# Performance work log

Hardware: AMD Instinct MI355X
Metric: run time of the kernel (lower is better)

## Reference

```python
import jax, jax.numpy as jnp
import numpy as np

HIDDEN = 1024

def setup_inputs() -> dict:
    key = jax.random.key(0)
    ks = jax.random.split(key, 7)
    B, S, H = 4, 2048, HIDDEN
    scale = 1.0 / np.sqrt(H)
    x = jax.random.normal(ks[0], (B, S, H), dtype=jnp.float32)
    Wq = jax.random.normal(ks[1], (H, H), dtype=jnp.float32) * scale
    Wk = jax.random.normal(ks[2], (H, H), dtype=jnp.float32) * scale
    Wv = jax.random.normal(ks[3], (H, H), dtype=jnp.float32) * scale
    bq = jax.random.normal(ks[4], (H,), dtype=jnp.float32) * 0.01
    bk = jax.random.normal(ks[5], (H,), dtype=jnp.float32) * 0.01
    bv = jax.random.normal(ks[6], (H,), dtype=jnp.float32) * 0.01
    return {"x": x, "Wq": Wq, "bq": bq, "Wk": Wk, "bk": bk, "Wv": Wv, "bv": bv}

def reference(x, Wq, bq, Wk, bk, Wv, bv):
    H = x.shape[-1]
    # Linear layers: y = x @ W^T + b (torch convention)
    Q = jnp.einsum('bsh,oh->bso', x, Wq) + bq
    K = jnp.einsum('bsh,oh->bso', x, Wk) + bk
    V = jnp.einsum('bsh,oh->bso', x, Wv) + bv
    # full O(S^2) score matrix, scaled by sqrt(hidden_dim) as in the source
    scores = jnp.einsum('bqh,bkh->bqk', Q, K) / jnp.sqrt(jnp.asarray(H, x.dtype))
    weights = jax.nn.softmax(scores, axis=-1)  # dropout is identity at inference
    out = jnp.einsum('bqk,bkh->bqh', weights, V)
    return out
```

## Files before the change

kernel.cpp:

```cpp
#include <hip/hip_runtime.h>
#include <hip/hip_bf16.h>

typedef __attribute__((ext_vector_type(8))) short bf16x8;
typedef __attribute__((ext_vector_type(4))) float f32x4;
typedef unsigned short u16;
typedef unsigned int u32;


__device__ __forceinline__ u16 f2bf(float f) {
  union { float f; u32 u; } v; v.f = f;
  u32 r = v.u + 0x7FFFu + ((v.u >> 16) & 1u);
  return (u16)(r >> 16);
}

__device__ __forceinline__ void gload_lds16(const u16* g, u16* l) {
  __builtin_amdgcn_global_load_lds(
      (const __attribute__((address_space(1))) u32*)(const void*)g,
      (__attribute__((address_space(3))) u32*)(void*)l, 16, 0, 0);
}


__global__ __launch_bounds__(256) void cvt_all(const float* __restrict__ x,
                                               const float* __restrict__ wq,
                                               const float* __restrict__ wk,
                                               const float* __restrict__ wv,
                                               u16* __restrict__ xb,
                                               u16* __restrict__ wcat) {
  const int bid = blockIdx.x;
  const float* src; u16* dst; size_t base;
  if (bid < 4096) { src = x; dst = xb; base = (size_t)bid * 2048; }
  else {
    int w = bid - 4096, s = w >> 9;
    src = (s == 0) ? wq : ((s == 1) ? wk : wv);
    dst = wcat + (size_t)s * 1048576;
    base = (size_t)(w & 511) * 2048;
  }
  size_t i = base + (size_t)threadIdx.x * 8;
  const float4* p = (const float4*)(src + i);
  float4 a = p[0], b = p[1];
  union { u16 u[8]; uint4 v; } r;
  r.u[0] = f2bf(a.x); r.u[1] = f2bf(a.y); r.u[2] = f2bf(a.z); r.u[3] = f2bf(a.w);
  r.u[4] = f2bf(b.x); r.u[5] = f2bf(b.y); r.u[6] = f2bf(b.z); r.u[7] = f2bf(b.w);
  *(uint4*)(dst + i) = r.v;
}


template<int MODE, int BM, int BN>
__global__ __launch_bounds__(512, 2) void gemm_pipe(
    const u16* __restrict__ A, const u16* __restrict__ B,
    const float* __restrict__ b0, const float* __restrict__ b1,
    const float* __restrict__ b2,
    void* __restrict__ o0, void* __restrict__ o1, void* __restrict__ o2,
    float* __restrict__ lsum, int lda, int ldb, int nkt,
    long Abat, long Bbat) {
  extern __shared__ u16 lds[];
  constexpr int NMT = BM / 32;
  constexpr int ANL = BM / 64;
  constexpr int BNL = BN / 64;
  constexpr int ASZ = BM * 64, BSZ = BN * 64;

  const int tid = threadIdx.x;
  const int lane = tid & 63, wv = tid >> 6;
  const int lr = lane & 15, lg = lane >> 4;
  const int wm = wv >> 2, wn = wv & 3;
  const int bm = blockIdx.x * BM, bn = blockIdx.y * BN;
  const int bz = blockIdx.z;

  const u16* Ab; const u16* Bb;
  if constexpr (MODE == 3) {
    Ab = A;
    Bb = B + (size_t)Bbat * (bm >> 11);
  } else {
    Ab = A + (size_t)Abat * bz;
    Bb = B + (size_t)Bbat * bz;
  }

  f32x4 acc[NMT][4];
#pragma unroll
  for (int i = 0; i < NMT; ++i)
#pragma unroll
    for (int j = 0; j < 4; ++j) acc[i][j] = (f32x4)0.0f;

  auto stage = [&](int kt, int buf) {
    u16* As = lds + buf * (ASZ + BSZ);
    u16* Bs = As + ASZ;
    const int k0 = kt * 64;
#pragma unroll
    for (int j = 0; j < ANL; ++j) {
      int id = j * 512 + tid, row = id >> 3, c = id & 7, cg = c ^ (row & 7);
      gload_lds16(Ab + (size_t)(bm + row) * lda + k0 + cg * 8, As + id * 8);
    }
#pragma unroll
    for (int j = 0; j < BNL; ++j) {
      int id = j * 512 + tid, row = id >> 3, c = id & 7, cg = c ^ (row & 7);
      gload_lds16(Bb + (size_t)(bn + row) * ldb + k0 + cg * 8, Bs + id * 8);
    }
  };

  stage(0, 0);
  __syncthreads();

  for (int kt = 0; kt < nkt; ++kt) {
    if (kt + 1 < nkt) stage(kt + 1, (kt + 1) & 1);
    __builtin_amdgcn_sched_barrier(0);
    const u16* As = lds + (kt & 1) * (ASZ + BSZ);
    const u16* Bs = As + ASZ;
#pragma unroll
    for (int kk = 0; kk < 2; ++kk) {
      bf16x8 a[NMT], b[4];
#pragma unroll
      for (int mt = 0; mt < NMT; ++mt) {
        int row = wm * (BM / 2) + mt * 16 + lr;
        int kc = (kk * 4 + lg) ^ (row & 7);
        a[mt] = *(const bf16x8*)(As + row * 64 + kc * 8);
      }
#pragma unroll
      for (int nt = 0; nt < 4; ++nt) {
        int row = wn * 64 + nt * 16 + lr;
        int kc = (kk * 4 + lg) ^ (row & 7);
        b[nt] = *(const bf16x8*)(Bs + row * 64 + kc * 8);
      }
#pragma unroll
      for (int mt = 0; mt < NMT; ++mt)
#pragma unroll
        for (int nt = 0; nt < 4; ++nt)
          acc[mt][nt] = __builtin_amdgcn_mfma_f32_16x16x32_bf16(a[mt], b[nt], acc[mt][nt], 0, 0, 0);
    }
    __syncthreads();
  }

  if constexpr (MODE == 0) {
    const int sel = bn >> 10;
    if (sel < 2) {
      const float* bp = sel ? b1 : b0;
      u16* o = sel ? (u16*)o1 : (u16*)o0;
#pragma unroll
      for (int nt = 0; nt < 4; ++nt) {
        int gcol = bn + wn * 64 + nt * 16 + lr;
        int col = gcol & 1023;
        float bv = bp[col];
#pragma unroll
        for (int mt = 0; mt < NMT; ++mt) {
          int grow0 = bm + wm * (BM / 2) + mt * 16 + lg * 4;
#pragma unroll
          for (int r = 0; r < 4; ++r)
            o[(size_t)(grow0 + r) * 1024 + col] = f2bf(acc[mt][nt][r] + bv);
        }
      }
    } else {
      u16* T = lds;
      const int col0 = bn - 2048;
      const int batch = bm >> 11;
      const int sbase = bm & 2047;
#pragma unroll
      for (int nt = 0; nt < 4; ++nt) {
        int col = wn * 64 + nt * 16 + lr;
        float bv = b2[col0 + col];
#pragma unroll
        for (int mt = 0; mt < NMT; ++mt) {
          int row0 = wm * (BM / 2) + mt * 16 + lg * 4;
#pragma unroll
          for (int r = 0; r < 4; ++r) {
            int row = row0 + r;
            T[row * 256 + (col ^ (((row >> 2) & 7) << 3))] = f2bf(acc[mt][nt][r] + bv);
          }
        }
      }
      __syncthreads();
      u16* o = (u16*)o2 + ((size_t)batch * 1024 + col0) * 2048 + sbase;
#pragma unroll
      for (int it = 0; it < 16; ++it) {
        int col = wv * 32 + (lane >> 2) + (it & 1) * 16;
        int s0 = ((it >> 1) * 4 + (lane & 3)) * 8;
        union { u16 u[8]; uint4 v; } pk;
#pragma unroll
        for (int k = 0; k < 8; ++k) {
          int row = s0 + k;
          pk.u[k] = T[row * 256 + (col ^ (((row >> 2) & 7) << 3))];
        }
        *(uint4*)(o + (size_t)col * 2048 + s0) = pk.v;
      }
    }
  } else if constexpr (MODE == 2) {
    u16* P = (u16*)o0 + (size_t)2048 * 2048 * bz;
    float psum[NMT][4];
#pragma unroll
    for (int mt = 0; mt < NMT; ++mt)
#pragma unroll
      for (int r = 0; r < 4; ++r) psum[mt][r] = 0.0f;
#pragma unroll
    for (int nt = 0; nt < 4; ++nt) {
      int gcol = bn + wn * 64 + nt * 16 + lr;
#pragma unroll
      for (int mt = 0; mt < NMT; ++mt) {
        int grow0 = bm + wm * (BM / 2) + mt * 16 + lg * 4;
#pragma unroll
        for (int r = 0; r < 4; ++r) {
          float e = __expf(acc[mt][nt][r] * 0.03125f);
          P[(size_t)(grow0 + r) * 2048 + gcol] = f2bf(e);
          psum[mt][r] += e;
        }
      }
    }
#pragma unroll
    for (int mt = 0; mt < NMT; ++mt)
#pragma unroll
      for (int r = 0; r < 4; ++r) {
#pragma unroll
        for (int off = 1; off < 16; off <<= 1)
          psum[mt][r] += __shfl_xor(psum[mt][r], off);
      }
    if (lr == 0) {
#pragma unroll
      for (int mt = 0; mt < NMT; ++mt) {
        int grow0 = bm + wm * (BM / 2) + mt * 16 + lg * 4;
#pragma unroll
        for (int r = 0; r < 4; ++r)
          atomicAdd(&lsum[bz * 2048 + grow0 + r], psum[mt][r]);
      }
    }
  } else {
    float* o = (float*)o0;
#pragma unroll
    for (int mt = 0; mt < NMT; ++mt) {
      int grow0 = bm + wm * (BM / 2) + mt * 16 + lg * 4;
      float inv[4];
#pragma unroll
      for (int r = 0; r < 4; ++r) inv[r] = 1.0f / lsum[grow0 + r];
#pragma unroll
      for (int nt = 0; nt < 4; ++nt) {
        int gcol = bn + wn * 64 + nt * 16 + lr;
#pragma unroll
        for (int r = 0; r < 4; ++r)
          o[(size_t)(grow0 + r) * 1024 + gcol] = acc[mt][nt][r] * inv[r];
      }
    }
  }
}


extern "C" void kernel_launch(void* const* d_in, const int* in_sizes, int n_in,
                              void* d_out, int out_size, void* d_ws, size_t ws_size,
                              hipStream_t stream) {
  const float* x  = (const float*)d_in[0];
  const float* Wq = (const float*)d_in[1];
  const float* bq = (const float*)d_in[2];
  const float* Wk = (const float*)d_in[3];
  const float* bk = (const float*)d_in[4];
  const float* Wv = (const float*)d_in[5];
  const float* bv = (const float*)d_in[6];
  float* out = (float*)d_out;

  char* ws = (char*)d_ws;
  u16*   xb   = (u16*)  (ws + ((size_t)0  << 20));
  u16*   wcat = (u16*)  (ws + ((size_t)16 << 20));
  float* lvec = (float*)(ws + ((size_t)23 << 20));
  u16*   qb   = (u16*)  (ws + ((size_t)24 << 20));
  u16*   kb   = (u16*)  (ws + ((size_t)40 << 20));
  u16*   vtb  = (u16*)  (ws + ((size_t)56 << 20));
  u16*   Pb   = (u16*)  (ws + ((size_t)72 << 20));

  hipFuncSetAttribute((const void*)&gemm_pipe<0, 256, 256>,
                      hipFuncAttributeMaxDynamicSharedMemorySize, 131072);
  hipFuncSetAttribute((const void*)&gemm_pipe<2, 256, 256>,
                      hipFuncAttributeMaxDynamicSharedMemorySize, 131072);
  hipFuncSetAttribute((const void*)&gemm_pipe<3, 128, 256>,
                      hipFuncAttributeMaxDynamicSharedMemorySize, 98304);

  hipMemsetAsync(lvec, 0, 8192 * sizeof(float), stream);
  cvt_all<<<dim3(5632), dim3(256), 0, stream>>>(x, Wq, Wk, Wv, xb, wcat);

  gemm_pipe<0, 256, 256><<<dim3(32, 12, 1), dim3(512), 131072, stream>>>(
      xb, wcat, bq, bk, bv, qb, kb, vtb, nullptr, 1024, 1024, 16, 0, 0);

  gemm_pipe<2, 256, 256><<<dim3(8, 8, 4), dim3(512), 131072, stream>>>(
      qb, kb, nullptr, nullptr, nullptr, Pb, nullptr, nullptr, lvec,
      1024, 1024, 16, (long)2048 * 1024, (long)2048 * 1024);

  gemm_pipe<3, 128, 256><<<dim3(64, 4, 1), dim3(512), 98304, stream>>>(
      Pb, vtb, nullptr, nullptr, nullptr, out, nullptr, nullptr, lvec,
      2048, 2048, 32, 0, (long)1024 * 2048);
}
```

Baseline: 246.1 us.

## Restructure GEMM main loop into eight-phase interleaved load/MFMA pipeline

Replaces the double-buffered GEMM loop with a finer schedule. Each 64-wide K tile is split into two 32-wide half slots, and the next tile's A and B loads are issued in four pieces interleaved with MFMA phases over two halves of the M tile. Explicit vmcnt/lgkmcnt waits, raw s_barrier and s_setprio replace the per-tile __syncthreads, so global-to-LDS copies overlap with matrix math. The LDS layout drops the XOR swizzle in favour of 32-element rows, which may bring back bank conflicts, and the hand-tuned waitcnt counts are fragile.

Result: slower. 269.7 us (+9.6%).

```diff
diff --git a/kernel.cpp b/kernel.cpp
--- a/kernel.cpp
+++ b/kernel.cpp
@@ -45,8 +45,8 @@
 }
 
 
-template<int MODE, int BM, int BN>
-__global__ __launch_bounds__(512, 2) void gemm_pipe(
+template<int MODE, int BM>
+__global__ __launch_bounds__(512, 2) void gemm8(
     const u16* __restrict__ A, const u16* __restrict__ B,
     const float* __restrict__ b0, const float* __restrict__ b1,
     const float* __restrict__ b2,
@@ -54,79 +54,109 @@
     float* __restrict__ lsum, int lda, int ldb, int nkt,
     long Abat, long Bbat) {
   extern __shared__ u16 lds[];
-  constexpr int NMT = BM / 32;
-  constexpr int ANL = BM / 64;
-  constexpr int BNL = BN / 64;
-  constexpr int ASZ = BM * 64, BSZ = BN * 64;
+  constexpr int MT = BM / 64;
+  constexpr int ASLOT = BM * 32;
+  constexpr int BSLOT = 256 * 32;
+  constexpr int BUFSZ = 2 * ASLOT + 2 * BSLOT;
+  constexpr int ALD = BM / 128;
 
   const int tid = threadIdx.x;
   const int lane = tid & 63, wv = tid >> 6;
   const int lr = lane & 15, lg = lane >> 4;
   const int wm = wv >> 2, wn = wv & 3;
-  const int bm = blockIdx.x * BM, bn = blockIdx.y * BN;
+  const int bm = blockIdx.x * BM, bn = blockIdx.y * 256;
   const int bz = blockIdx.z;
 
   const u16* Ab; const u16* Bb;
-  if constexpr (MODE == 3) {
-    Ab = A;
-    Bb = B + (size_t)Bbat * (bm >> 11);
-  } else {
-    Ab = A + (size_t)Abat * bz;
-    Bb = B + (size_t)Bbat * bz;
-  }
-
-  f32x4 acc[NMT][4];
-#pragma unroll
-  for (int i = 0; i < NMT; ++i)
+  if constexpr (MODE == 3) { Ab = A; Bb = B + (size_t)Bbat * (bm >> 11); }
+  else { Ab = A + (size_t)Abat * bz; Bb = B + (size_t)Bbat * bz; }
+
+  f32x4 acc[2 * MT][4];
+#pragma unroll
+  for (int i = 0; i < 2 * MT; ++i)
 #pragma unroll
     for (int j = 0; j < 4; ++j) acc[i][j] = (f32x4)0.0f;
 
-  auto stage = [&](int kt, int buf) {
-    u16* As = lds + buf * (ASZ + BSZ);
-    u16* Bs = As + ASZ;
-    const int k0 = kt * 64;
-#pragma unroll
-    for (int j = 0; j < ANL; ++j) {
-      int id = j * 512 + tid, row = id >> 3, c = id & 7, cg = c ^ (row & 7);
-      gload_lds16(Ab + (size_t)(bm + row) * lda + k0 + cg * 8, As + id * 8);
-    }
-#pragma unroll
-    for (int j = 0; j < BNL; ++j) {
-      int id = j * 512 + tid, row = id >> 3, c = id & 7, cg = c ^ (row & 7);
-      gload_lds16(Bb + (size_t)(bn + row) * ldb + k0 + cg * 8, Bs + id * 8);
+  auto stageA = [&](int t1, int ks) {
+    u16* base = lds + (t1 & 1) * BUFSZ + ks * ASLOT;
+    const int k0 = t1 * 64 + ks * 32;
+#pragma unroll
+    for (int j = 0; j < ALD; ++j) {
+      int id = j * 512 + tid, row = id >> 2, kg = id & 3;
+      gload_lds16(Ab + (size_t)(bm + row) * lda + k0 + kg * 8, base + id * 8);
     }
   };
-
-  stage(0, 0);
-  __syncthreads();
-
-  for (int kt = 0; kt < nkt; ++kt) {
-    if (kt + 1 < nkt) stage(kt + 1, (kt + 1) & 1);
-    __builtin_amdgcn_sched_barrier(0);
-    const u16* As = lds + (kt & 1) * (ASZ + BSZ);
-    const u16* Bs = As + ASZ;
-#pragma unroll
-    for (int kk = 0; kk < 2; ++kk) {
-      bf16x8 a[NMT], b[4];
-#pragma unroll
-      for (int mt = 0; mt < NMT; ++mt) {
-        int row = wm * (BM / 2) + mt * 16 + lr;
-        int kc = (kk * 4 + lg) ^ (row & 7);
-        a[mt] = *(const bf16x8*)(As + row * 64 + kc * 8);
-      }
-#pragma unroll
-      for (int nt = 0; nt < 4; ++nt) {
-        int row = wn * 64 + nt * 16 + lr;
-        int kc = (kk * 4 + lg) ^ (row & 7);
-        b[nt] = *(const bf16x8*)(Bs + row * 64 + kc * 8);
-      }
-#pragma unroll
-      for (int mt = 0; mt < NMT; ++mt)
-#pragma unroll
-        for (int nt = 0; nt < 4; ++nt)
-          acc[mt][nt] = __builtin_amdgcn_mfma_f32_16x16x32_bf16(a[mt], b[nt], acc[mt][nt], 0, 0, 0);
-    }
-    __syncthreads();
+  auto stageB = [&](int t1, int ks) {
+    u16* base = lds + (t1 & 1) * BUFSZ + 2 * ASLOT + ks * BSLOT;
+    const int k0 = t1 * 64 + ks * 32;
+#pragma unroll
+    for (int j = 0; j < 2; ++j) {
+      int id = j * 512 + tid, row = id >> 2, kg = id & 3;
+      gload_lds16(Bb + (size_t)(bn + row) * ldb + k0 + kg * 8, base + id * 8);
+    }
+  };
+
+  stageA(0, 0); stageB(0, 0); stageA(0, 1); stageB(0, 1);
+  if constexpr (BM == 256) asm volatile("s_waitcnt vmcnt(4)" ::: "memory");
+  else                     asm volatile("s_waitcnt vmcnt(3)" ::: "memory");
+  __builtin_amdgcn_s_barrier();
+
+  for (int t = 0; t < nkt; ++t) {
+    const bool stg = (t + 1 < nkt);
+    const u16* Ab0 = lds + (t & 1) * BUFSZ;
+    const u16* Bb0 = Ab0 + 2 * ASLOT;
+    bf16x8 bfr[4];
+#pragma unroll
+    for (int ks = 0; ks < 2; ++ks) {
+#pragma unroll
+      for (int mh = 0; mh < 2; ++mh) {
+        if (mh == 0) {
+#pragma unroll
+          for (int nt = 0; nt < 4; ++nt) {
+            int row = wn * 64 + nt * 16 + lr;
+            bfr[nt] = *(const bf16x8*)(Bb0 + ks * BSLOT + row * 32 + lg * 8);
+          }
+        }
+        bf16x8 afr[MT];
+#pragma unroll
+        for (int mt = 0; mt < MT; ++mt) {
+          int row = wm * (BM / 2) + mh * (BM / 4) + mt * 16 + lr;
+          afr[mt] = *(const bf16x8*)(Ab0 + ks * ASLOT + row * 32 + lg * 8);
+        }
+        if (stg) {
+          if (ks == 0 && mh == 0) stageA(t + 1, 0);
+          else if (ks == 0 && mh == 1) stageB(t + 1, 0);
+          else if (ks == 1 && mh == 0) stageA(t + 1, 1);
+          else stageB(t + 1, 1);
+        }
+        __builtin_amdgcn_s_barrier();
+        asm volatile("s_waitcnt lgkmcnt(0)" ::: "memory");
+        __builtin_amdgcn_sched_barrier(0);
+        __builtin_amdgcn_s_setprio(1);
+#pragma unroll
+        for (int mt = 0; mt < MT; ++mt)
+#pragma unroll
+          for (int nt = 0; nt < 4; ++nt)
+            acc[mh * MT + mt][nt] = __builtin_amdgcn_mfma_f32_16x16x32_bf16(
+                afr[mt], bfr[nt], acc[mh * MT + mt][nt], 0, 0, 0);
+        __builtin_amdgcn_s_setprio(0);
+        __builtin_amdgcn_sched_barrier(0);
+        if (mh == 1) {
+          if (ks == 0) {
+            if (stg) {
+              if constexpr (BM == 256) asm volatile("s_waitcnt vmcnt(4)" ::: "memory");
+              else                     asm volatile("s_waitcnt vmcnt(3)" ::: "memory");
+            } else {
+              asm volatile("s_waitcnt vmcnt(0)" ::: "memory");
+            }
+          } else if (stg) {
+            if constexpr (BM == 256) asm volatile("s_waitcnt vmcnt(4)" ::: "memory");
+            else                     asm volatile("s_waitcnt vmcnt(3)" ::: "memory");
+          }
+        }
+        __builtin_amdgcn_s_barrier();
+      }
+    }
   }
 
   if constexpr (MODE == 0) {
@@ -136,16 +166,17 @@
       u16* o = sel ? (u16*)o1 : (u16*)o0;
 #pragma unroll
       for (int nt = 0; nt < 4; ++nt) {
-        int gcol = bn + wn * 64 + nt * 16 + lr;
-        int col = gcol & 1023;
+        int col = (bn + wn * 64 + nt * 16 + lr) & 1023;
         float bv = bp[col];
 #pragma unroll
-        for (int mt = 0; mt < NMT; ++mt) {
-          int grow0 = bm + wm * (BM / 2) + mt * 16 + lg * 4;
-#pragma unroll
-          for (int r = 0; r < 4; ++r)
-            o[(size_t)(grow0 + r) * 1024 + col] = f2bf(acc[mt][nt][r] + bv);
-        }
+        for (int mh = 0; mh < 2; ++mh)
+#pragma unroll
+          for (int mt = 0; mt < MT; ++mt) {
+            int grow0 = bm + wm * (BM / 2) + mh * (BM / 4) + mt * 16 + lg * 4;
+#pragma unroll
+            for (int r = 0; r < 4; ++r)
+              o[(size_t)(grow0 + r) * 1024 + col] = f2bf(acc[mh * MT + mt][nt][r] + bv);
+          }
       }
     } else {
       u16* T = lds;
@@ -157,14 +188,16 @@
         int col = wn * 64 + nt * 16 + lr;
         float bv = b2[col0 + col];
 #pragma unroll
-        for (int mt = 0; mt < NMT; ++mt) {
-          int row0 = wm * (BM / 2) + mt * 16 + lg * 4;
-#pragma unroll
-          for (int r = 0; r < 4; ++r) {
-            int row = row0 + r;
-            T[row * 256 + (col ^ (((row >> 2) & 7) << 3))] = f2bf(acc[mt][nt][r] + bv);
+        for (int mh = 0; mh < 2; ++mh)
+#pragma unroll
+          for (int mt = 0; mt < MT; ++mt) {
+            int row0 = wm * (BM / 2) + mh * (BM / 4) + mt * 16 + lg * 4;
+#pragma unroll
+            for (int r = 0; r < 4; ++r) {
+              int row = row0 + r;
+              T[row * 256 + (col ^ (((row >> 2) & 7) << 3))] = f2bf(acc[mh * MT + mt][nt][r] + bv);
+            }
           }
-        }
       }
       __syncthreads();
       u16* o = (u16*)o2 + ((size_t)batch * 1024 + col0) * 2048 + sbase;
@@ -183,47 +216,47 @@
     }
   } else if constexpr (MODE == 2) {
     u16* P = (u16*)o0 + (size_t)2048 * 2048 * bz;
-    float psum[NMT][4];
-#pragma unroll
-    for (int mt = 0; mt < NMT; ++mt)
-#pragma unroll
-      for (int r = 0; r < 4; ++r) psum[mt][r] = 0.0f;
+    float psum[2 * MT][4];
+#pragma unroll
+    for (int i = 0; i < 2 * MT; ++i)
+#pragma unroll
+      for (int r = 0; r < 4; ++r) psum[i][r] = 0.0f;
 #pragma unroll
     for (int nt = 0; nt < 4; ++nt) {
       int gcol = bn + wn * 64 + nt * 16 + lr;
 #pragma unroll
-      for (int mt = 0; mt < NMT; ++mt) {
-        int grow0 = bm + wm * (BM / 2) + mt * 16 + lg * 4;
+      for (int i = 0; i < 2 * MT; ++i) {
+        int grow0 = bm + wm * (BM / 2) + (i / MT) * (BM / 4) + (i % MT) * 16 + lg * 4;
 #pragma unroll
         for (int r = 0; r < 4; ++r) {
-          float e = __expf(acc[mt][nt][r] * 0.03125f);
+          float e = __expf(acc[i][nt][r] * 0.03125f);
           P[(size_t)(grow0 + r) * 2048 + gcol] = f2bf(e);
-          psum[mt][r] += e;
-        }
-      }
-    }
-#pragma unroll
-    for (int mt = 0; mt < NMT; ++mt)
+          psum[i][r] += e;
+        }
+      }
+    }
+#pragma unroll
+    for (int i = 0; i < 2 * MT; ++i)
 #pragma unroll
       for (int r = 0; r < 4; ++r) {
 #pragma unroll
         for (int off = 1; off < 16; off <<= 1)
-          psum[mt][r] += __shfl_xor(psum[mt][r], off);
+          psum[i][r] += __shfl_xor(psum[i][r], off);
       }
     if (lr == 0) {
 #pragma unroll
-      for (int mt = 0; mt < NMT; ++mt) {
-        int grow0 = bm + wm * (BM / 2) + mt * 16 + lg * 4;
+      for (int i = 0; i < 2 * MT; ++i) {
+        int grow0 = bm + wm * (BM / 2) + (i / MT) * (BM / 4) + (i % MT) * 16 + lg * 4;
 #pragma unroll
         for (int r = 0; r < 4; ++r)
-          atomicAdd(&lsum[bz * 2048 + grow0 + r], psum[mt][r]);
+          atomicAdd(&lsum[bz * 2048 + grow0 + r], psum[i][r]);
       }
     }
   } else {
     float* o = (float*)o0;
 #pragma unroll
-    for (int mt = 0; mt < NMT; ++mt) {
-      int grow0 = bm + wm * (BM / 2) + mt * 16 + lg * 4;
+    for (int i = 0; i < 2 * MT; ++i) {
+      int grow0 = bm + wm * (BM / 2) + (i / MT) * (BM / 4) + (i % MT) * 16 + lg * 4;
       float inv[4];
 #pragma unroll
       for (int r = 0; r < 4; ++r) inv[r] = 1.0f / lsum[grow0 + r];
@@ -232,7 +265,7 @@
         int gcol = bn + wn * 64 + nt * 16 + lr;
 #pragma unroll
         for (int r = 0; r < 4; ++r)
-          o[(size_t)(grow0 + r) * 1024 + gcol] = acc[mt][nt][r] * inv[r];
+          o[(size_t)(grow0 + r) * 1024 + gcol] = acc[i][nt][r] * inv[r];
       }
     }
   }
@@ -260,24 +293,24 @@
   u16*   vtb  = (u16*)  (ws + ((size_t)56 << 20));
   u16*   Pb   = (u16*)  (ws + ((size_t)72 << 20));
 
-  hipFuncSetAttribute((const void*)&gemm_pipe<0, 256, 256>,
+  hipFuncSetAttribute((const void*)&gemm8<0, 256>,
                       hipFuncAttributeMaxDynamicSharedMemorySize, 131072);
-  hipFuncSetAttribute((const void*)&gemm_pipe<2, 256, 256>,
+  hipFuncSetAttribute((const void*)&gemm8<2, 256>,
                       hipFuncAttributeMaxDynamicSharedMemorySize, 131072);
-  hipFuncSetAttribute((const void*)&gemm_pipe<3, 128, 256>,
+  hipFuncSetAttribute((const void*)&gemm8<3, 128>,
                       hipFuncAttributeMaxDynamicSharedMemorySize, 98304);
 
   hipMemsetAsync(lvec, 0, 8192 * sizeof(float), stream);
   cvt_all<<<dim3(5632), dim3(256), 0, stream>>>(x, Wq, Wk, Wv, xb, wcat);
 
-  gemm_pipe<0, 256, 256><<<dim3(32, 12, 1), dim3(512), 131072, stream>>>(
+  gemm8<0, 256><<<dim3(32, 12, 1), dim3(512), 131072, stream>>>(
       xb, wcat, bq, bk, bv, qb, kb, vtb, nullptr, 1024, 1024, 16, 0, 0);
 
-  gemm_pipe<2, 256, 256><<<dim3(8, 8, 4), dim3(512), 131072, stream>>>(
+  gemm8<2, 256><<<dim3(8, 8, 4), dim3(512), 131072, stream>>>(
       qb, kb, nullptr, nullptr, nullptr, Pb, nullptr, nullptr, lvec,
       1024, 1024, 16, (long)2048 * 1024, (long)2048 * 1024);
 
-  gemm_pipe<3, 128, 256><<<dim3(64, 4, 1), dim3(512), 98304, stream>>>(
+  gemm8<3, 128><<<dim3(64, 4, 1), dim3(512), 98304, stream>>>(
       Pb, vtb, nullptr, nullptr, nullptr, out, nullptr, nullptr, lvec,
       2048, 2048, 32, 0, (long)1024 * 2048);
 }
```

## Replace double-buffered 256-tile GEMMs with single-buffered 128x128 tiles and fold memset

Applied to the files above, without the earlier changes.

Replaces the 512-thread, 256x256 double-buffered GEMM template with a 256-thread 128x128 kernel that uses static 32KB shared memory and no prefetch pipelining. Grids grow to 1536, 1024 and 512 blocks so the 256 CUs get more blocks and more resident waves. The memset of the row-sum vector moves into an extra block of the convert kernel, which removes one launch. The trade-off is lower arithmetic intensity per tile, which roughly doubles LDS/global traffic per FLOP, and no overlap of loads with MFMA inside a block.

New measurement: 263.5 us. 7.1% more time.

```diff
diff --git a/kernel.cpp b/kernel.cpp
--- a/kernel.cpp
+++ b/kernel.cpp
@@ -25,8 +25,16 @@
                                                const float* __restrict__ wk,
                                                const float* __restrict__ wv,
                                                u16* __restrict__ xb,
-                                               u16* __restrict__ wcat) {
+                                               u16* __restrict__ wcat,
+                                               float* __restrict__ lvec) {
   const int bid = blockIdx.x;
+  if (bid == 5632) {
+    float4 z = make_float4(0.f, 0.f, 0.f, 0.f);
+#pragma unroll
+    for (int j = 0; j < 8; ++j)
+      *(float4*)(lvec + (j * 256 + threadIdx.x) * 4) = z;
+    return;
+  }
   const float* src; u16* dst; size_t base;
   if (bid < 4096) { src = x; dst = xb; base = (size_t)bid * 2048; }
   else {
@@ -45,83 +53,62 @@
 }
 
 
-template<int MODE, int BM, int BN>
-__global__ __launch_bounds__(512, 2) void gemm_pipe(
+template<int MODE>
+__global__ __launch_bounds__(256) void gemm128(
     const u16* __restrict__ A, const u16* __restrict__ B,
     const float* __restrict__ b0, const float* __restrict__ b1,
     const float* __restrict__ b2,
     void* __restrict__ o0, void* __restrict__ o1, void* __restrict__ o2,
     float* __restrict__ lsum, int lda, int ldb, int nkt,
     long Abat, long Bbat) {
-  extern __shared__ u16 lds[];
-  constexpr int NMT = BM / 32;
-  constexpr int ANL = BM / 64;
-  constexpr int BNL = BN / 64;
-  constexpr int ASZ = BM * 64, BSZ = BN * 64;
-
+  __shared__ u16 smem[16384];
+  u16* As = smem;
+  u16* Bs = smem + 8192;
   const int tid = threadIdx.x;
   const int lane = tid & 63, wv = tid >> 6;
   const int lr = lane & 15, lg = lane >> 4;
-  const int wm = wv >> 2, wn = wv & 3;
-  const int bm = blockIdx.x * BM, bn = blockIdx.y * BN;
+  const int wm = (wv >> 1) * 64, wn = (wv & 1) * 64;
+  const int bm = blockIdx.x * 128, bn = blockIdx.y * 128;
   const int bz = blockIdx.z;
 
   const u16* Ab; const u16* Bb;
-  if constexpr (MODE == 3) {
-    Ab = A;
-    Bb = B + (size_t)Bbat * (bm >> 11);
-  } else {
-    Ab = A + (size_t)Abat * bz;
-    Bb = B + (size_t)Bbat * bz;
-  }
-
-  f32x4 acc[NMT][4];
-#pragma unroll
-  for (int i = 0; i < NMT; ++i)
+  if constexpr (MODE == 3) { Ab = A; Bb = B + (size_t)Bbat * (bm >> 11); }
+  else { Ab = A + (size_t)Abat * bz; Bb = B + (size_t)Bbat * bz; }
+
+  f32x4 acc[4][4];
+#pragma unroll
+  for (int i = 0; i < 4; ++i)
 #pragma unroll
     for (int j = 0; j < 4; ++j) acc[i][j] = (f32x4)0.0f;
 
-  auto stage = [&](int kt, int buf) {
-    u16* As = lds + buf * (ASZ + BSZ);
-    u16* Bs = As + ASZ;
+  for (int kt = 0; kt < nkt; ++kt) {
     const int k0 = kt * 64;
 #pragma unroll
-    for (int j = 0; j < ANL; ++j) {
-      int id = j * 512 + tid, row = id >> 3, c = id & 7, cg = c ^ (row & 7);
+    for (int i = 0; i < 4; ++i) {
+      int id = i * 256 + tid;
+      int row = id >> 3, c = id & 7;
+      int cg = c ^ (row & 7);
       gload_lds16(Ab + (size_t)(bm + row) * lda + k0 + cg * 8, As + id * 8);
-    }
-#pragma unroll
-    for (int j = 0; j < BNL; ++j) {
-      int id = j * 512 + tid, row = id >> 3, c = id & 7, cg = c ^ (row & 7);
       gload_lds16(Bb + (size_t)(bn + row) * ldb + k0 + cg * 8, Bs + id * 8);
     }
-  };
-
-  stage(0, 0);
-  __syncthreads();
-
-  for (int kt = 0; kt < nkt; ++kt) {
-    if (kt + 1 < nkt) stage(kt + 1, (kt + 1) & 1);
-    __builtin_amdgcn_sched_barrier(0);
-    const u16* As = lds + (kt & 1) * (ASZ + BSZ);
-    const u16* Bs = As + ASZ;
+    __syncthreads();
 #pragma unroll
     for (int kk = 0; kk < 2; ++kk) {
-      bf16x8 a[NMT], b[4];
-#pragma unroll
-      for (int mt = 0; mt < NMT; ++mt) {
-        int row = wm * (BM / 2) + mt * 16 + lr;
+      bf16x8 a[4], b[4];
+#pragma unroll
+      for (int mt = 0; mt < 4; ++mt) {
+        int row = wm + mt * 16 + lr;
         int kc = (kk * 4 + lg) ^ (row & 7);
         a[mt] = *(const bf16x8*)(As + row * 64 + kc * 8);
       }
 #pragma unroll
       for (int nt = 0; nt < 4; ++nt) {
-        int row = wn * 64 + nt * 16 + lr;
+        int row = wn + nt * 16 + lr;
         int kc = (kk * 4 + lg) ^ (row & 7);
         b[nt] = *(const bf16x8*)(Bs + row * 64 + kc * 8);
       }
 #pragma unroll
-      for (int mt = 0; mt < NMT; ++mt)
+      for (int mt = 0; mt < 4; ++mt)
 #pragma unroll
         for (int nt = 0; nt < 4; ++nt)
           acc[mt][nt] = __builtin_amdgcn_mfma_f32_16x16x32_bf16(a[mt], b[nt], acc[mt][nt], 0, 0, 0);
@@ -136,64 +123,63 @@
       u16* o = sel ? (u16*)o1 : (u16*)o0;
 #pragma unroll
       for (int nt = 0; nt < 4; ++nt) {
-        int gcol = bn + wn * 64 + nt * 16 + lr;
-        int col = gcol & 1023;
+        int col = (bn + wn + nt * 16 + lr) & 1023;
         float bv = bp[col];
 #pragma unroll
-        for (int mt = 0; mt < NMT; ++mt) {
-          int grow0 = bm + wm * (BM / 2) + mt * 16 + lg * 4;
+        for (int mt = 0; mt < 4; ++mt) {
+          int grow0 = bm + wm + mt * 16 + lg * 4;
 #pragma unroll
           for (int r = 0; r < 4; ++r)
             o[(size_t)(grow0 + r) * 1024 + col] = f2bf(acc[mt][nt][r] + bv);
         }
       }
     } else {
-      u16* T = lds;
+      u16* T = smem;
       const int col0 = bn - 2048;
       const int batch = bm >> 11;
       const int sbase = bm & 2047;
 #pragma unroll
       for (int nt = 0; nt < 4; ++nt) {
-        int col = wn * 64 + nt * 16 + lr;
+        int col = wn + nt * 16 + lr;
         float bv = b2[col0 + col];
 #pragma unroll
-        for (int mt = 0; mt < NMT; ++mt) {
-          int row0 = wm * (BM / 2) + mt * 16 + lg * 4;
+        for (int mt = 0; mt < 4; ++mt) {
+          int row0 = wm + mt * 16 + lg * 4;
 #pragma unroll
           for (int r = 0; r < 4; ++r) {
             int row = row0 + r;
-            T[row * 256 + (col ^ (((row >> 2) & 7) << 3))] = f2bf(acc[mt][nt][r] + bv);
+            T[row * 128 + (col ^ (((row >> 2) & 7) << 3))] = f2bf(acc[mt][nt][r] + bv);
           }
         }
       }
       __syncthreads();
       u16* o = (u16*)o2 + ((size_t)batch * 1024 + col0) * 2048 + sbase;
 #pragma unroll
-      for (int it = 0; it < 16; ++it) {
+      for (int it = 0; it < 8; ++it) {
         int col = wv * 32 + (lane >> 2) + (it & 1) * 16;
         int s0 = ((it >> 1) * 4 + (lane & 3)) * 8;
         union { u16 u[8]; uint4 v; } pk;
 #pragma unroll
         for (int k = 0; k < 8; ++k) {
           int row = s0 + k;
-          pk.u[k] = T[row * 256 + (col ^ (((row >> 2) & 7) << 3))];
+          pk.u[k] = T[row * 128 + (col ^ (((row >> 2) & 7) << 3))];
         }
         *(uint4*)(o + (size_t)col * 2048 + s0) = pk.v;
       }
     }
   } else if constexpr (MODE == 2) {
     u16* P = (u16*)o0 + (size_t)2048 * 2048 * bz;
-    float psum[NMT][4];
-#pragma unroll
-    for (int mt = 0; mt < NMT; ++mt)
+    float psum[4][4];
+#pragma unroll
+    for (int mt = 0; mt < 4; ++mt)
 #pragma unroll
       for (int r = 0; r < 4; ++r) psum[mt][r] = 0.0f;
 #pragma unroll
     for (int nt = 0; nt < 4; ++nt) {
-      int gcol = bn + wn * 64 + nt * 16 + lr;
-#pragma unroll
-      for (int mt = 0; mt < NMT; ++mt) {
-        int grow0 = bm + wm * (BM / 2) + mt * 16 + lg * 4;
+      int gcol = bn + wn + nt * 16 + lr;
+#pragma unroll
+      for (int mt = 0; mt < 4; ++mt) {
+        int grow0 = bm + wm + mt * 16 + lg * 4;
 #pragma unroll
         for (int r = 0; r < 4; ++r) {
           float e = __expf(acc[mt][nt][r] * 0.03125f);
@@ -203,7 +189,7 @@
       }
     }
 #pragma unroll
-    for (int mt = 0; mt < NMT; ++mt)
+    for (int mt = 0; mt < 4; ++mt)
 #pragma unroll
       for (int r = 0; r < 4; ++r) {
 #pragma unroll
@@ -212,8 +198,8 @@
       }
     if (lr == 0) {
 #pragma unroll
-      for (int mt = 0; mt < NMT; ++mt) {
-        int grow0 = bm + wm * (BM / 2) + mt * 16 + lg * 4;
+      for (int mt = 0; mt < 4; ++mt) {
+        int grow0 = bm + wm + mt * 16 + lg * 4;
 #pragma unroll
         for (int r = 0; r < 4; ++r)
           atomicAdd(&lsum[bz * 2048 + grow0 + r], psum[mt][r]);
@@ -222,14 +208,14 @@
   } else {
     float* o = (float*)o0;
 #pragma unroll
-    for (int mt = 0; mt < NMT; ++mt) {
-      int grow0 = bm + wm * (BM / 2) + mt * 16 + lg * 4;
+    for (int mt = 0; mt < 4; ++mt) {
+      int grow0 = bm + wm + mt * 16 + lg * 4;
       float inv[4];
 #pragma unroll
       for (int r = 0; r < 4; ++r) inv[r] = 1.0f / lsum[grow0 + r];
 #pragma unroll
       for (int nt = 0; nt < 4; ++nt) {
-        int gcol = bn + wn * 64 + nt * 16 + lr;
+        int gcol = bn + wn + nt * 16 + lr;
 #pragma unroll
         for (int r = 0; r < 4; ++r)
           o[(size_t)(grow0 + r) * 1024 + gcol] = acc[mt][nt][r] * inv[r];
@@ -260,24 +246,16 @@
   u16*   vtb  = (u16*)  (ws + ((size_t)56 << 20));
   u16*   Pb   = (u16*)  (ws + ((size_t)72 << 20));
 
-  hipFuncSetAttribute((const void*)&gemm_pipe<0, 256, 256>,
-                      hipFuncAttributeMaxDynamicSharedMemorySize, 131072);
-  hipFuncSetAttribute((const void*)&gemm_pipe<2, 256, 256>,
-                      hipFuncAttributeMaxDynamicSharedMemorySize, 131072);
-  hipFuncSetAttribute((const void*)&gemm_pipe<3, 128, 256>,
-                      hipFuncAttributeMaxDynamicSharedMemorySize, 98304);
-
-  hipMemsetAsync(lvec, 0, 8192 * sizeof(float), stream);
-  cvt_all<<<dim3(5632), dim3(256), 0, stream>>>(x, Wq, Wk, Wv, xb, wcat);
-
-  gemm_pipe<0, 256, 256><<<dim3(32, 12, 1), dim3(512), 131072, stream>>>(
+  cvt_all<<<dim3(5633), dim3(256), 0, stream>>>(x, Wq, Wk, Wv, xb, wcat, lvec);
+
+  gemm128<0><<<dim3(64, 24, 1), dim3(256), 0, stream>>>(
       xb, wcat, bq, bk, bv, qb, kb, vtb, nullptr, 1024, 1024, 16, 0, 0);
 
-  gemm_pipe<2, 256, 256><<<dim3(8, 8, 4), dim3(512), 131072, stream>>>(
+  gemm128<2><<<dim3(16, 16, 4), dim3(256), 0, stream>>>(
       qb, kb, nullptr, nullptr, nullptr, Pb, nullptr, nullptr, lvec,
       1024, 1024, 16, (long)2048 * 1024, (long)2048 * 1024);
 
-  gemm_pipe<3, 128, 256><<<dim3(64, 4, 1), dim3(512), 98304, stream>>>(
+  gemm128<3><<<dim3(64, 8, 1), dim3(256), 0, stream>>>(
       Pb, vtb, nullptr, nullptr, nullptr, out, nullptr, nullptr, lvec,
       2048, 2048, 32, 0, (long)1024 * 2048);
 }
```
